# Kernel tuning notes

Hardware: AMD Instinct MI355X
Metric: run time of the kernel (lower is better)

## Reference

```python
import jax, jax.numpy as jnp
import numpy as np

D_MODEL = 1024
NUM_HEADS = 16
HEAD_DIM = D_MODEL // NUM_HEADS


def setup_inputs() -> dict:
    key = jax.random.key(0)
    ks = jax.random.split(key, 9)
    s = 1.0 / np.sqrt(D_MODEL)
    x = jax.random.normal(ks[0], (4, 2048, D_MODEL), dtype=jnp.float32)
    Wq = jax.random.uniform(ks[1], (D_MODEL, D_MODEL), jnp.float32, -s, s)
    bq = jax.random.uniform(ks[2], (D_MODEL,), jnp.float32, -s, s)
    Wk = jax.random.uniform(ks[3], (D_MODEL, D_MODEL), jnp.float32, -s, s)
    bk = jax.random.uniform(ks[4], (D_MODEL,), jnp.float32, -s, s)
    Wv = jax.random.uniform(ks[5], (D_MODEL, D_MODEL), jnp.float32, -s, s)
    bv = jax.random.uniform(ks[6], (D_MODEL,), jnp.float32, -s, s)
    Wo = jax.random.uniform(ks[7], (D_MODEL, D_MODEL), jnp.float32, -s, s)
    bo = jax.random.uniform(ks[8], (D_MODEL,), jnp.float32, -s, s)
    return {"x": x, "Wq": Wq, "bq": bq, "Wk": Wk, "bk": bk,
            "Wv": Wv, "bv": bv, "Wo": Wo, "bo": bo}


def reference(x, Wq, bq, Wk, bk, Wv, bv, Wo, bo):
    B, S, D = x.shape
    H, hd = NUM_HEADS, HEAD_DIM
    # QKV projections (torch Linear: x @ W^T + b)
    q = (x @ Wq.T + bq).reshape(B, S, H, hd).transpose(0, 2, 1, 3)  # [B,H,S,hd]
    k = (x @ Wk.T + bk).reshape(B, S, H, hd).transpose(0, 2, 1, 3)
    v = (x @ Wv.T + bv).reshape(B, S, H, hd).transpose(0, 2, 1, 3)
    scores = jnp.einsum('bhqd,bhkd->bhqk', q, k) / jnp.sqrt(jnp.float32(hd))
    attn = jax.nn.softmax(scores, axis=-1)  # dropout is identity in eval
    ctx = jnp.einsum('bhqk,bhkd->bhqd', attn, v)
    ctx = ctx.transpose(0, 2, 1, 3).reshape(B, S, D)
    return ctx @ Wo.T + bo
```

## Files before the change

### kernel.cpp

```cpp
#include <hip/hip_runtime.h>

typedef __bf16 bf16;
typedef __bf16 bf16x4 __attribute__((ext_vector_type(4)));
typedef __bf16 bf16x8 __attribute__((ext_vector_type(8)));
typedef float  f32x4  __attribute__((ext_vector_type(4)));
typedef float  f32x16 __attribute__((ext_vector_type(16)));
typedef unsigned int u32x4v __attribute__((ext_vector_type(4)));

#define NB   4
#define SEQ  2048
#define DM   1024
#define NH   16
#define HD   64
#define BHN  (NB*NH)
#define MTOT (NB*SEQ)
#define ELEMS ((size_t)MTOT*DM)
#define WELEMS (DM*DM)
#define QSCALE 0.18033688011112042f

__device__ __forceinline__ void gload16(void* lds, const void* g) {
  __builtin_amdgcn_global_load_lds(
      (const __attribute__((address_space(1))) void*)g,
      (__attribute__((address_space(3))) void*)lds, 16, 0, 0);
}

__device__ __forceinline__ f32x4 mfma16(bf16x8 a, bf16x8 b, f32x4 c) {
  return __builtin_amdgcn_mfma_f32_16x16x32_bf16(a, b, c, 0, 0, 0);
}
__device__ __forceinline__ f32x16 mfma32(bf16x8 a, bf16x8 b, f32x16 c) {
  return __builtin_amdgcn_mfma_f32_32x32x16_bf16(a, b, c, 0, 0, 0);
}
__device__ __forceinline__ unsigned cvtpk(float lo, float hi) {
  unsigned r;
  asm("v_cvt_pk_bf16_f32 %0, %1, %2" : "=v"(r) : "v"(lo), "v"(hi));
  return r;
}
__device__ __forceinline__ float exp2a(float x) {
  float r;
  asm("v_exp_f32 %0, %1" : "=v"(r) : "v"(x));
  return r;
}

__global__ __launch_bounds__(256) void cvt_all(
    const float* __restrict__ x, bf16* __restrict__ xb,
    const float* __restrict__ w0, const float* __restrict__ w1,
    const float* __restrict__ w2, const float* __restrict__ w3,
    bf16* __restrict__ wb)
{
  int y = blockIdx.y;
  const float* src; bf16* dst; int nblk;
  if (y < 4) {
    src = (y == 0) ? w0 : (y == 1) ? w1 : (y == 2) ? w2 : w3;
    dst = wb + (size_t)y * WELEMS;
    nblk = WELEMS / 1024;
  } else {
    src = x; dst = xb; nblk = (int)(ELEMS / 1024);
  }
  if (blockIdx.x >= nblk) return;
  int i = blockIdx.x * 1024 + threadIdx.x * 4;
  f32x4 v = *(const f32x4*)(src + i);
  bf16x4 o;
#pragma unroll
  for (int j = 0; j < 4; j++) o[j] = (bf16)v[j];
  *(bf16x4*)(dst + i) = o;
}

#define GEMM_CORE(A_, W_)                                                      \
  __shared__ __align__(16) bf16 lds_a[128*32];                                 \
  __shared__ __align__(16) bf16 lds_b[128*32];                                 \
  const int K = 1024;                                                          \
  int tid = threadIdx.x, wid = tid >> 6, lane = tid & 63;                      \
  int m0 = blockIdx.y * 128, n0 = blockIdx.x * 128;                            \
  int wr = wid >> 1, wc = wid & 1;                                             \
  int c15 = lane & 15, hi = lane >> 4;                                         \
  int srow = lane >> 2, scol = (lane & 3) * 8;                                 \
  const bf16* gA = (A_) + (m0 + wid*32 + srow) * K + scol;                     \
  const bf16* gB = (W_) + (n0 + wid*32 + srow) * K + scol;                     \
  bf16* la = lds_a + wid*1024;                                                 \
  bf16* lb = lds_b + wid*1024;                                                 \
  f32x4 acc[4][4] = {};                                                        \
  for (int k0 = 0; k0 < K; k0 += 32) {                                         \
    __syncthreads();                                                           \
    gload16(la,       gA + k0);                                                \
    gload16(la + 512, gA + 16*K + k0);                                         \
    gload16(lb,       gB + k0);                                                \
    gload16(lb + 512, gB + 16*K + k0);                                         \
    __syncthreads();                                                           \
    bf16x8 af[4], bfr[4];                                                      \
    _Pragma("unroll")                                                          \
    for (int i = 0; i < 4; i++)                                                \
      af[i]  = *(const bf16x8*)(lds_a + (wr*64 + i*16 + c15)*32 + hi*8);       \
    _Pragma("unroll")                                                          \
    for (int i = 0; i < 4; i++)                                                \
      bfr[i] = *(const bf16x8*)(lds_b + (wc*64 + i*16 + c15)*32 + hi*8);       \
    _Pragma("unroll")                                                          \
    for (int mi = 0; mi < 4; mi++)                                             \
      _Pragma("unroll")                                                        \
      for (int ni = 0; ni < 4; ni++)                                           \
        acc[mi][ni] = mfma16(af[mi], bfr[ni], acc[mi][ni]);                    \
  }

__global__ __launch_bounds__(256) void gemm_qkv(
    const bf16* __restrict__ A, const bf16* __restrict__ Wb3,
    const float* __restrict__ bq, const float* __restrict__ bk,
    const float* __restrict__ bv,
    bf16* __restrict__ Qb, bf16* __restrict__ Kb, bf16* __restrict__ Vtb)
{
  int z = blockIdx.z;
  const bf16* W = Wb3 + (size_t)z * WELEMS;
  const float* bias = (z == 0) ? bq : (z == 1) ? bk : bv;
  GEMM_CORE(A, W)

  float sc = (z == 0) ? QSCALE : 1.0f;
#pragma unroll
  for (int mi = 0; mi < 4; mi++) {
#pragma unroll
    for (int ni = 0; ni < 4; ni++) {
      int col = n0 + wc*64 + ni*16 + c15;
      float bvv = bias[col];
      int row = m0 + wr*64 + mi*16 + hi*4;
      int b = row >> 11, s = row & 2047;
      int h = col >> 6,  d = col & 63;
      if (z < 2) {
        bf16* C = z ? Kb : Qb;
#pragma unroll
        for (int r = 0; r < 4; r++)
          C[((b*NH + h)*SEQ + (s + r))*HD + d] = (bf16)((acc[mi][ni][r] + bvv) * sc);
      } else {
        bf16x4 o;
#pragma unroll
        for (int r = 0; r < 4; r++) o[r] = (bf16)(acc[mi][ni][r] + bvv);
        *(bf16x4*)(Vtb + ((size_t)(b*NH + h)*HD + d)*SEQ + s) = o;
      }
    }
  }
}

__global__ __launch_bounds__(256) void gemm_out(
    const bf16* __restrict__ A, const bf16* __restrict__ W,
    const float* __restrict__ bias, float* __restrict__ C)
{
  GEMM_CORE(A, W)
#pragma unroll
  for (int mi = 0; mi < 4; mi++) {
#pragma unroll
    for (int ni = 0; ni < 4; ni++) {
      int col = n0 + wc*64 + ni*16 + c15;
      float bvv = bias[col];
      int row = m0 + wr*64 + mi*16 + hi*4;
#pragma unroll
      for (int r = 0; r < 4; r++)
        C[(row + r)*DM + col] = acc[mi][ni][r] + bvv;
    }
  }
}

__global__ __launch_bounds__(256, 2) void attn(
    const bf16* __restrict__ Q, const bf16* __restrict__ Kin,
    const bf16* __restrict__ Vt, bf16* __restrict__ ctx)
{
  __shared__ __align__(16) bf16 kt[3][64*64];
  __shared__ __align__(16) bf16 vt[3][64*64];

  int tid = threadIdx.x, wid = tid >> 6, lane = tid & 63;
  int l31 = lane & 31, hi = lane >> 5, l7 = lane & 7;

  int orig = blockIdx.y * gridDim.x + blockIdx.x;
  int swz  = (orig & 7) * 64 + (orig >> 3);
  int bh   = swz >> 3, q0 = (swz & 7) * 256;

  const bf16* Qp = Q   + (size_t)bh*SEQ*HD;
  const bf16* Kp = Kin + (size_t)bh*SEQ*HD;
  const bf16* Vp = Vt  + (size_t)bh*HD*SEQ;
  int qw = q0 + wid*64;

  bf16x8 qf[2][4];
#pragma unroll
  for (int qt = 0; qt < 2; qt++)
#pragma unroll
    for (int dblk = 0; dblk < 4; dblk++)
      qf[qt][dblk] = *(const bf16x8*)(Qp + (size_t)(qw + qt*32 + l31)*HD + dblk*16 + hi*8);

  f32x16 po[2][2] = {};
  f32x16 posum[2] = {};

  bf16x8 onesv;
#pragma unroll
  for (int j = 0; j < 8; j++) onesv[j] = (bf16)1.0f;

  int r8 = lane >> 3;
  int c16s = (lane & 7) ^ r8;

#define STAGE(buf, kv0)                                                        \
  {                                                                            \
    _Pragma("unroll")                                                          \
    for (int op = 0; op < 2; op++) {                                           \
      int rowl = wid*16 + op*8 + r8;                                           \
      gload16(&kt[buf][(wid*16 + op*8)*64], Kp + (size_t)((kv0) + rowl)*HD + c16s*8); \
      gload16(&vt[buf][(wid*16 + op*8)*64], Vp + (size_t)rowl*SEQ + (kv0) + c16s*8);  \
    }                                                                          \
  }

  const int NT = SEQ / 64;
  STAGE(0, 0);
  STAGE(1, 64);

  int cur = 0;
  for (int it = 0; it < NT; ++it) {
    if (it < NT - 1) { asm volatile("s_waitcnt vmcnt(4)" ::: "memory"); }
    else             { asm volatile("s_waitcnt vmcnt(0)" ::: "memory"); }
    __builtin_amdgcn_s_barrier();
    asm volatile("" ::: "memory");
    if (it + 2 < NT) {
      int sb = (cur >= 1) ? cur - 1 : 2;
      STAGE(sb, (it + 2) * 64);
    }

    f32x16 st[2][2] = {};
    __builtin_amdgcn_s_setprio(1);
#pragma unroll
    for (int kvt = 0; kvt < 2; kvt++) {
      int rowb = (kvt*32 + l31) * 64;
#pragma unroll
      for (int dblk = 0; dblk < 4; dblk++) {
        bf16x8 kf = *(const bf16x8*)(&kt[cur][rowb + (((dblk*2 + hi) ^ l7) * 8)]);
        st[0][kvt] = mfma32(kf, qf[0][dblk], st[0][kvt]);
        st[1][kvt] = mfma32(kf, qf[1][dblk], st[1][kvt]);
      }
    }
    __builtin_amdgcn_s_setprio(0);

    bf16x8 pa[2][2][2];
#pragma unroll
    for (int qt = 0; qt < 2; qt++) {
#pragma unroll
      for (int kvt = 0; kvt < 2; kvt++)
#pragma unroll
        for (int i = 0; i < 16; i++)
          st[qt][kvt][i] = exp2a(st[qt][kvt][i]);
#pragma unroll
      for (int kvt = 0; kvt < 2; kvt++)
#pragma unroll
        for (int cp = 0; cp < 2; cp++) {
          int m0 = 2*cp, m1 = 2*cp + 1;
          unsigned w0a = cvtpk(st[qt][kvt][4*m0+0], st[qt][kvt][4*m0+1]);
          unsigned w1a = cvtpk(st[qt][kvt][4*m0+2], st[qt][kvt][4*m0+3]);
          unsigned w0b = cvtpk(st[qt][kvt][4*m1+0], st[qt][kvt][4*m1+1]);
          unsigned w1b = cvtpk(st[qt][kvt][4*m1+2], st[qt][kvt][4*m1+3]);
          asm("v_permlane32_swap_b32 %0, %1" : "+v"(w0a), "+v"(w0b));
          asm("v_permlane32_swap_b32 %0, %1" : "+v"(w1a), "+v"(w1b));
          pa[qt][kvt][cp] = __builtin_bit_cast(bf16x8, (u32x4v){w0a, w1a, w0b, w1b});
        }
    }

    __builtin_amdgcn_s_setprio(1);
#pragma unroll
    for (int dt = 0; dt < 2; dt++) {
      int rowb = (dt*32 + l31) * 64;
#pragma unroll
      for (int c = 0; c < 4; c++) {
        bf16x8 vf = *(const bf16x8*)(&vt[cur][rowb + (((c*2 + hi) ^ l7) * 8)]);
        po[0][dt] = mfma32(pa[0][c >> 1][c & 1], vf, po[0][dt]);
        po[1][dt] = mfma32(pa[1][c >> 1][c & 1], vf, po[1][dt]);
      }
    }
#pragma unroll
    for (int c = 0; c < 4; c++) {
      posum[0] = mfma32(pa[0][c >> 1][c & 1], onesv, posum[0]);
      posum[1] = mfma32(pa[1][c >> 1][c & 1], onesv, posum[1]);
    }
    __builtin_amdgcn_s_setprio(0);

    cur = (cur == 2) ? 0 : cur + 1;
  }
#undef STAGE

  int b = bh >> 4, h = bh & 15;
#pragma unroll
  for (int qt = 0; qt < 2; qt++)
#pragma unroll
    for (int reg = 0; reg < 16; reg++) {
      int qq = (reg & 3) + 8*(reg >> 2) + 4*hi;
      float inv = 1.0f / posum[qt][reg];
      int s = qw + qt*32 + qq;
      bf16* dst = ctx + (size_t)(b*SEQ + s)*DM + h*HD + l31;
      dst[0]  = (bf16)(po[qt][0][reg] * inv);
      dst[32] = (bf16)(po[qt][1][reg] * inv);
    }
}

extern "C" void kernel_launch(void* const* d_in, const int* in_sizes, int n_in,
                              void* d_out, int out_size, void* d_ws, size_t ws_size,
                              hipStream_t stream)
{
  const float* x  = (const float*)d_in[0];
  const float* Wq = (const float*)d_in[1];
  const float* bq = (const float*)d_in[2];
  const float* Wk = (const float*)d_in[3];
  const float* bk = (const float*)d_in[4];
  const float* Wv = (const float*)d_in[5];
  const float* bv = (const float*)d_in[6];
  const float* Wo = (const float*)d_in[7];
  const float* bo = (const float*)d_in[8];

  bf16* ws  = (bf16*)d_ws;
  bf16* xb  = ws;
  bf16* Wb  = ws + ELEMS;
  bf16* Qb  = ws + ELEMS + 4*WELEMS;
  bf16* Kb  = Qb + ELEMS;
  bf16* Vtb = Kb + ELEMS;
  bf16* ctx = xb;

  dim3 blk(256);

  cvt_all<<<dim3(ELEMS/1024, 5), blk, 0, stream>>>(x, xb, Wq, Wk, Wv, Wo, Wb);
  gemm_qkv<<<dim3(DM/128, MTOT/128, 3), blk, 0, stream>>>(
      xb, Wb, bq, bk, bv, Qb, Kb, Vtb);
  attn<<<dim3(SEQ/256, BHN), blk, 0, stream>>>(Qb, Kb, Vtb, ctx);
  gemm_out<<<dim3(DM/128, MTOT/128), blk, 0, stream>>>(
      ctx, Wb + 3*WELEMS, bo, (float*)d_out);
}
```

Baseline: 190.8 us.

## Software-pipeline QK and softmax/PV across KV tiles, replace ones-MFMA row sums

Restructures the attention loop so the QK^T MFMAs of tile i+1 are issued before the exp/convert/PV work of tile i, using two score register sets and a 4-deep LDS ring. This lets the exp and VALU packing overlap with matrix-core work. It also drops the extra MFMAs against a ones vector for the softmax denominator and sums the bf16 probabilities with VALU instead, combined by cross-lane shuffles at the end. The cost is more registers for the doubled score buffers and more LDS, which may hurt occupancy at 2 blocks per CU.

Result: slower. 203.5 us (+6.6%).

```diff
diff --git a/kernel.cpp b/kernel.cpp
--- a/kernel.cpp
+++ b/kernel.cpp
@@ -155,12 +155,89 @@
   }
 }
 
+__device__ __forceinline__ void qk_phase(
+    f32x16 (&st)[2][2], const bf16* __restrict__ ktb,
+    const bf16x8 (&qf)[2][4], int l31, int hi, int l7)
+{
+  f32x16 zz = {};
+  __builtin_amdgcn_s_setprio(1);
+#pragma unroll
+  for (int kvt = 0; kvt < 2; kvt++) {
+    int rowb = (kvt*32 + l31) * 64;
+    {
+      bf16x8 kf = *(const bf16x8*)(ktb + rowb + (((0*2 + hi) ^ l7) * 8));
+      st[0][kvt] = mfma32(kf, qf[0][0], zz);
+      st[1][kvt] = mfma32(kf, qf[1][0], zz);
+    }
+#pragma unroll
+    for (int dblk = 1; dblk < 4; dblk++) {
+      bf16x8 kf = *(const bf16x8*)(ktb + rowb + (((dblk*2 + hi) ^ l7) * 8));
+      st[0][kvt] = mfma32(kf, qf[0][dblk], st[0][kvt]);
+      st[1][kvt] = mfma32(kf, qf[1][dblk], st[1][kvt]);
+    }
+  }
+  __builtin_amdgcn_s_setprio(0);
+}
+
+__device__ __forceinline__ void sm_pv_phase(
+    f32x16 (&st)[2][2], const bf16* __restrict__ vtb,
+    f32x16 (&po)[2][2], float (&lrun)[2], int l31, int hi, int l7)
+{
+  bf16x8 pa[2][2][2];
+#pragma unroll
+  for (int qt = 0; qt < 2; qt++) {
+#pragma unroll
+    for (int kvt = 0; kvt < 2; kvt++)
+#pragma unroll
+      for (int i = 0; i < 16; i++)
+        st[qt][kvt][i] = exp2a(st[qt][kvt][i]);
+#pragma unroll
+    for (int kvt = 0; kvt < 2; kvt++)
+#pragma unroll
+      for (int cp = 0; cp < 2; cp++) {
+        int m0 = 2*cp, m1 = 2*cp + 1;
+        unsigned w0a = cvtpk(st[qt][kvt][4*m0+0], st[qt][kvt][4*m0+1]);
+        unsigned w1a = cvtpk(st[qt][kvt][4*m0+2], st[qt][kvt][4*m0+3]);
+        unsigned w0b = cvtpk(st[qt][kvt][4*m1+0], st[qt][kvt][4*m1+1]);
+        unsigned w1b = cvtpk(st[qt][kvt][4*m1+2], st[qt][kvt][4*m1+3]);
+        asm("v_permlane32_swap_b32 %0, %1" : "+v"(w0a), "+v"(w0b));
+        asm("v_permlane32_swap_b32 %0, %1" : "+v"(w1a), "+v"(w1b));
+        pa[qt][kvt][cp] = __builtin_bit_cast(bf16x8, (u32x4v){w0a, w1a, w0b, w1b});
+      }
+    float rs = 0.f;
+#pragma unroll
+    for (int kvt = 0; kvt < 2; kvt++)
+#pragma unroll
+      for (int cp = 0; cp < 2; cp++) {
+        u32x4v w = __builtin_bit_cast(u32x4v, pa[qt][kvt][cp]);
+#pragma unroll
+        for (int j = 0; j < 4; j++) {
+          rs += __builtin_bit_cast(float, w[j] << 16);
+          rs += __builtin_bit_cast(float, w[j] & 0xffff0000u);
+        }
+      }
+    lrun[qt] += rs;
+  }
+  __builtin_amdgcn_s_setprio(1);
+#pragma unroll
+  for (int dt = 0; dt < 2; dt++) {
+    int rowb = (dt*32 + l31) * 64;
+#pragma unroll
+    for (int c = 0; c < 4; c++) {
+      bf16x8 vf = *(const bf16x8*)(vtb + rowb + (((c*2 + hi) ^ l7) * 8));
+      po[0][dt] = mfma32(pa[0][c >> 1][c & 1], vf, po[0][dt]);
+      po[1][dt] = mfma32(pa[1][c >> 1][c & 1], vf, po[1][dt]);
+    }
+  }
+  __builtin_amdgcn_s_setprio(0);
+}
+
 __global__ __launch_bounds__(256, 2) void attn(
     const bf16* __restrict__ Q, const bf16* __restrict__ Kin,
     const bf16* __restrict__ Vt, bf16* __restrict__ ctx)
 {
-  __shared__ __align__(16) bf16 kt[3][64*64];
-  __shared__ __align__(16) bf16 vt[3][64*64];
+  __shared__ __align__(16) bf16 kt[4][64*64];
+  __shared__ __align__(16) bf16 vt[4][64*64];
 
   int tid = threadIdx.x, wid = tid >> 6, lane = tid & 63;
   int l31 = lane & 31, hi = lane >> 5, l7 = lane & 7;
@@ -182,11 +259,8 @@
       qf[qt][dblk] = *(const bf16x8*)(Qp + (size_t)(qw + qt*32 + l31)*HD + dblk*16 + hi*8);
 
   f32x16 po[2][2] = {};
-  f32x16 posum[2] = {};
-
-  bf16x8 onesv;
-#pragma unroll
-  for (int j = 0; j < 8; j++) onesv[j] = (bf16)1.0f;
+  float lrun[2] = {0.f, 0.f};
+  f32x16 stA[2][2], stB[2][2];
 
   int r8 = lane >> 3;
   int c16s = (lane & 7) ^ r8;
@@ -201,92 +275,48 @@
     }                                                                          \
   }
 
+#define TOP(itv)                                                               \
+  {                                                                            \
+    if ((itv) < NT - 1) { asm volatile("s_waitcnt vmcnt(4)" ::: "memory"); }   \
+    else                { asm volatile("s_waitcnt vmcnt(0)" ::: "memory"); }   \
+    __builtin_amdgcn_s_barrier();                                              \
+    asm volatile("" ::: "memory");                                             \
+    if ((itv) + 2 < NT) STAGE(((itv) + 2) & 3, ((itv) + 2) * 64);              \
+  }
+
   const int NT = SEQ / 64;
   STAGE(0, 0);
   STAGE(1, 64);
 
-  int cur = 0;
-  for (int it = 0; it < NT; ++it) {
-    if (it < NT - 1) { asm volatile("s_waitcnt vmcnt(4)" ::: "memory"); }
-    else             { asm volatile("s_waitcnt vmcnt(0)" ::: "memory"); }
-    __builtin_amdgcn_s_barrier();
-    asm volatile("" ::: "memory");
-    if (it + 2 < NT) {
-      int sb = (cur >= 1) ? cur - 1 : 2;
-      STAGE(sb, (it + 2) * 64);
-    }
-
-    f32x16 st[2][2] = {};
-    __builtin_amdgcn_s_setprio(1);
-#pragma unroll
-    for (int kvt = 0; kvt < 2; kvt++) {
-      int rowb = (kvt*32 + l31) * 64;
-#pragma unroll
-      for (int dblk = 0; dblk < 4; dblk++) {
-        bf16x8 kf = *(const bf16x8*)(&kt[cur][rowb + (((dblk*2 + hi) ^ l7) * 8)]);
-        st[0][kvt] = mfma32(kf, qf[0][dblk], st[0][kvt]);
-        st[1][kvt] = mfma32(kf, qf[1][dblk], st[1][kvt]);
-      }
-    }
-    __builtin_amdgcn_s_setprio(0);
-
-    bf16x8 pa[2][2][2];
-#pragma unroll
-    for (int qt = 0; qt < 2; qt++) {
-#pragma unroll
-      for (int kvt = 0; kvt < 2; kvt++)
-#pragma unroll
-        for (int i = 0; i < 16; i++)
-          st[qt][kvt][i] = exp2a(st[qt][kvt][i]);
-#pragma unroll
-      for (int kvt = 0; kvt < 2; kvt++)
-#pragma unroll
-        for (int cp = 0; cp < 2; cp++) {
-          int m0 = 2*cp, m1 = 2*cp + 1;
-          unsigned w0a = cvtpk(st[qt][kvt][4*m0+0], st[qt][kvt][4*m0+1]);
-          unsigned w1a = cvtpk(st[qt][kvt][4*m0+2], st[qt][kvt][4*m0+3]);
-          unsigned w0b = cvtpk(st[qt][kvt][4*m1+0], st[qt][kvt][4*m1+1]);
-          unsigned w1b = cvtpk(st[qt][kvt][4*m1+2], st[qt][kvt][4*m1+3]);
-          asm("v_permlane32_swap_b32 %0, %1" : "+v"(w0a), "+v"(w0b));
-          asm("v_permlane32_swap_b32 %0, %1" : "+v"(w1a), "+v"(w1b));
-          pa[qt][kvt][cp] = __builtin_bit_cast(bf16x8, (u32x4v){w0a, w1a, w0b, w1b});
-        }
-    }
-
-    __builtin_amdgcn_s_setprio(1);
-#pragma unroll
-    for (int dt = 0; dt < 2; dt++) {
-      int rowb = (dt*32 + l31) * 64;
-#pragma unroll
-      for (int c = 0; c < 4; c++) {
-        bf16x8 vf = *(const bf16x8*)(&vt[cur][rowb + (((c*2 + hi) ^ l7) * 8)]);
-        po[0][dt] = mfma32(pa[0][c >> 1][c & 1], vf, po[0][dt]);
-        po[1][dt] = mfma32(pa[1][c >> 1][c & 1], vf, po[1][dt]);
-      }
-    }
-#pragma unroll
-    for (int c = 0; c < 4; c++) {
-      posum[0] = mfma32(pa[0][c >> 1][c & 1], onesv, posum[0]);
-      posum[1] = mfma32(pa[1][c >> 1][c & 1], onesv, posum[1]);
-    }
-    __builtin_amdgcn_s_setprio(0);
-
-    cur = (cur == 2) ? 0 : cur + 1;
-  }
+  for (int itb = 0; itb < NT; itb += 2) {
+    TOP(itb)
+    qk_phase(stA, &kt[itb & 3][0], qf, l31, hi, l7);
+    if (itb > 0)
+      sm_pv_phase(stB, &vt[(itb - 1) & 3][0], po, lrun, l31, hi, l7);
+
+    TOP(itb + 1)
+    qk_phase(stB, &kt[(itb + 1) & 3][0], qf, l31, hi, l7);
+    sm_pv_phase(stA, &vt[itb & 3][0], po, lrun, l31, hi, l7);
+  }
+  sm_pv_phase(stB, &vt[(NT - 1) & 3][0], po, lrun, l31, hi, l7);
 #undef STAGE
+#undef TOP
 
   int b = bh >> 4, h = bh & 15;
 #pragma unroll
-  for (int qt = 0; qt < 2; qt++)
+  for (int qt = 0; qt < 2; qt++) {
+    float lf  = lrun[qt] + __shfl_xor(lrun[qt], 32, 64);
+    float inv = 1.0f / lf;
 #pragma unroll
     for (int reg = 0; reg < 16; reg++) {
       int qq = (reg & 3) + 8*(reg >> 2) + 4*hi;
-      float inv = 1.0f / posum[qt][reg];
+      float iq = __shfl(inv, qq, 64);
       int s = qw + qt*32 + qq;
       bf16* dst = ctx + (size_t)(b*SEQ + s)*DM + h*HD + l31;
-      dst[0]  = (bf16)(po[qt][0][reg] * inv);
-      dst[32] = (bf16)(po[qt][1][reg] * inv);
-    }
+      dst[0]  = (bf16)(po[qt][0][reg] * iq);
+      dst[32] = (bf16)(po[qt][1][reg] * iq);
+    }
+  }
 }
 
 extern "C" void kernel_launch(void* const* d_in, const int* in_sizes, int n_in,
```
